# Kernel tuning notes

Hardware: AMD Instinct MI355X
Metric: run time of the kernel (lower is better)

## Reference

```python
import jax, jax.numpy as jnp
import numpy as np

N = 100000   # nodes
E = 600000   # edges
K = 3        # TAGConv hops
EPS = 1e-5   # BatchNorm eps
SLOPE = 0.01 # LeakyReLU negative slope


def setup_inputs() -> dict:
    key = jax.random.key(0)
    ks = jax.random.split(key, 8)
    y = jax.random.normal(ks[0], (N, 128), dtype=jnp.float32)
    edge_index = jax.random.randint(ks[1], (2, E), 0, N, dtype=jnp.int64)
    edge_attr = jax.random.uniform(ks[2], (E,), dtype=jnp.float32)
    # TAGConv layer l has (K+1) weight matrices [in, out]; bias only on first two layers
    W1 = 0.1 * jax.random.normal(ks[3], (K + 1, 128, 128), dtype=jnp.float32)
    b1 = jnp.full((128,), 0.1, dtype=jnp.float32)
    W2 = 0.1 * jax.random.normal(ks[4], (K + 1, 128, 128), dtype=jnp.float32)
    b2 = jnp.full((128,), 0.1, dtype=jnp.float32)
    W3 = 0.1 * jax.random.normal(ks[5], (K + 1, 128, 64), dtype=jnp.float32)
    g1 = jnp.ones((128,), jnp.float32); be1 = jnp.zeros((128,), jnp.float32)
    g2 = jnp.ones((128,), jnp.float32); be2 = jnp.zeros((128,), jnp.float32)
    g3 = jnp.ones((64,), jnp.float32);  be3 = jnp.zeros((64,), jnp.float32)
    return dict(y=y, edge_index=edge_index, edge_attr=edge_attr,
                W1=W1, b1=b1, g1=g1, be1=be1,
                W2=W2, b2=b2, g2=g2, be2=be2,
                W3=W3, g3=g3, be3=be3)


def _tag_conv(x, W, b, src, dst, norm):
    # out = sum_{k=0..K} A_hat^k x @ W_k (+ b)
    out = x @ W[0]
    h = x
    for k in range(1, W.shape[0]):
        h = jax.ops.segment_sum(norm[:, None] * h[src], dst, num_segments=N)
        out = out + h @ W[k]
    return out if b is None else out + b


def _bn(x, g, b):
    # BatchNorm1d training mode: biased batch stats over nodes
    m = x.mean(axis=0)
    v = jnp.mean((x - m) ** 2, axis=0)
    return (x - m) * jax.lax.rsqrt(v + EPS) * g + b


def reference(y, edge_index, edge_attr, W1, b1, g1, be1, W2, b2, g2, be2, W3, g3, be3):
    src, dst = edge_index[0], edge_index[1]
    # gcn_norm (symmetric, no self-loops): D^{-1/2} A D^{-1/2}
    deg = jax.ops.segment_sum(edge_attr, dst, num_segments=N)
    dis = jnp.where(deg > 0, jax.lax.rsqrt(jnp.maximum(deg, 1e-12)), 0.0)
    norm = dis[src] * edge_attr * dis[dst]
    lrelu = lambda t: jax.nn.leaky_relu(t, SLOPE)
    x = lrelu(_bn(_tag_conv(y, W1, b1, src, dst, norm), g1, be1))
    x = lrelu(_bn(_tag_conv(x, W2, b2, src, dst, norm), g2, be2))
    x = lrelu(_bn(_tag_conv(x, W3, None, src, dst, norm), g3, be3))
    return x
```

## Files before the change

kernel.cpp:

```cpp
#include <hip/hip_runtime.h>
#include <hip/hip_bf16.h>

typedef unsigned short b16;
typedef __attribute__((ext_vector_type(8))) unsigned short us8;
typedef __attribute__((ext_vector_type(8))) short short8;
typedef __attribute__((ext_vector_type(4))) float float4v;

#define NN 100000
#define NE 600000

__device__ __forceinline__ float bf2f(b16 u) {
    return __uint_as_float(((unsigned)u) << 16);
}
__device__ __forceinline__ b16 f2bf(float f) {
    unsigned x = __float_as_uint(f);
    return (b16)((x + 0x7fffu + ((x >> 16) & 1u)) >> 16);
}

__global__ void k_detect(const void* __restrict__ y, const void* __restrict__ ei,
                         int* __restrict__ flags) {
    if (threadIdx.x == 0 && blockIdx.x == 0) {
        const b16* p = (const b16*)y;
        int f32 = 0;
        for (int i = 0; i < 128; ++i) {
            float v = bf2f(p[i]);
            if (!(fabsf(v) < 1e4f)) { f32 = 1; break; }
        }
        flags[0] = f32;
        const long long* q = (const long long*)ei;
        int i64 = 1;
        for (int i = 0; i < 4; ++i) {
            long long v = q[i];
            if (v < 0 || v >= NN) i64 = 0;
        }
        flags[1] = i64;
    }
}

__global__ void k_cvt(const void* __restrict__ in, float* __restrict__ out, int n,
                      const int* __restrict__ flags) {
    int i = blockIdx.x * blockDim.x + threadIdx.x;
    if (i >= n) return;
    out[i] = flags[0] ? ((const float*)in)[i] : bf2f(((const b16*)in)[i]);
}

__global__ void k_idx(const void* __restrict__ ei, int* __restrict__ src32,
                      int* __restrict__ dst32, const int* __restrict__ flags) {
    int e = blockIdx.x * blockDim.x + threadIdx.x;
    if (e >= NE) return;
    int s, d;
    if (flags[1]) {
        const long long* p = (const long long*)ei;
        s = (int)p[e];
        d = (int)p[NE + e];
    } else {
        const int* p = (const int*)ei;
        s = p[e];
        d = p[NE + e];
    }
    src32[e] = ((unsigned)s < NN) ? s : 0;
    dst32[e] = ((unsigned)d < NN) ? d : 0;
}

__global__ void k_degcnt(const int* __restrict__ dst, const void* __restrict__ ea,
                         float* __restrict__ deg, int* __restrict__ cnt,
                         const int* __restrict__ flags) {
    int e = blockIdx.x * blockDim.x + threadIdx.x;
    if (e >= NE) return;
    float w = flags[0] ? ((const float*)ea)[e] : bf2f(((const b16*)ea)[e]);
    int d = dst[e];
    unsafeAtomicAdd(&deg[d], w);
    atomicAdd(&cnt[d], 1);
}

__global__ void k_dis(float* deg) {
    int n = blockIdx.x * blockDim.x + threadIdx.x;
    if (n < NN) {
        float d = deg[n];
        deg[n] = (d > 0.f) ? rsqrtf(fmaxf(d, 1e-12f)) : 0.f;
    }
}

#define SCAN_B 1024
#define SCAN_NB ((NN + SCAN_B - 1) / SCAN_B)

__global__ __launch_bounds__(SCAN_B) void k_scan1(const int* __restrict__ cnt,
                                                  int* __restrict__ inc,
                                                  int* __restrict__ bsum) {
    __shared__ int s[SCAN_B];
    int i = blockIdx.x * SCAN_B + threadIdx.x;
    s[threadIdx.x] = (i < NN) ? cnt[i] : 0;
    __syncthreads();
    for (int off = 1; off < SCAN_B; off <<= 1) {
        int t = (threadIdx.x >= off) ? s[threadIdx.x - off] : 0;
        __syncthreads();
        s[threadIdx.x] += t;
        __syncthreads();
    }
    if (i < NN) inc[i] = s[threadIdx.x];
    if (threadIdx.x == SCAN_B - 1) bsum[blockIdx.x] = s[SCAN_B - 1];
}

__global__ void k_scan2(int* bsum) {
    if (threadIdx.x == 0 && blockIdx.x == 0) {
        int a = 0;
        for (int i = 0; i < SCAN_NB; ++i) {
            int t = bsum[i];
            bsum[i] = a;
            a += t;
        }
    }
}

__global__ void k_scan3(const int* __restrict__ inc, const int* __restrict__ bsum,
                        int* __restrict__ rowptr) {
    int i = blockIdx.x * blockDim.x + threadIdx.x;
    if (i == 0) rowptr[0] = 0;
    if (i < NN) rowptr[i + 1] = inc[i] + bsum[i / SCAN_B];
}

__global__ void k_fill(const int* __restrict__ src, const int* __restrict__ dst,
                       const void* __restrict__ ea, const float* __restrict__ dis,
                       const int* __restrict__ rowptr, int* __restrict__ fill,
                       int* __restrict__ csrc, float* __restrict__ cw,
                       const int* __restrict__ flags) {
    int e = blockIdx.x * blockDim.x + threadIdx.x;
    if (e >= NE) return;
    float a = flags[0] ? ((const float*)ea)[e] : bf2f(((const b16*)ea)[e]);
    int d = dst[e];
    int s = src[e];
    int pos = rowptr[d] + atomicAdd(&fill[d], 1);
    csrc[pos] = s;
    cw[pos] = dis[s] * a * dis[d];
}

__global__ void k_pack(const void* __restrict__ W, b16* __restrict__ Wp, int NC,
                       const int* __restrict__ flags) {
    int f = blockIdx.x * blockDim.x + threadIdx.x;
    int total = 512 * NC / 8;
    if (f >= total) return;
    int lane = f & 63;
    int rest = f >> 6;
    int CT = NC >> 4;
    int ct = rest % CT, ks = rest / CT;
    int k0 = 32 * ks + (lane >> 4) * 8;
    int col = 16 * ct + (lane & 15);
    us8 v;
#pragma unroll
    for (int j = 0; j < 8; ++j) {
        float x = flags[0] ? ((const float*)W)[(size_t)(k0 + j) * NC + col]
                           : bf2f(((const b16*)W)[(size_t)(k0 + j) * NC + col]);
        v[j] = f2bf(x);
    }
    *(us8*)&Wp[(size_t)f * 8] = v;
}

__global__ void k_cast(const void* __restrict__ y, b16* __restrict__ XC,
                       const int* __restrict__ flags) {
    int i = blockIdx.x * blockDim.x + threadIdx.x;
    if (i >= NN * 32) return;
    int row = i >> 5, cg = i & 31;
    float4 v;
    if (flags[0]) {
        v = ((const float4*)y)[i];
    } else {
        ushort4 u = ((const ushort4*)y)[i];
        v = make_float4(bf2f(u.x), bf2f(u.y), bf2f(u.z), bf2f(u.w));
    }
    ushort4 o;
    o.x = f2bf(v.x); o.y = f2bf(v.y); o.z = f2bf(v.z); o.w = f2bf(v.w);
    *(ushort4*)&XC[(size_t)row * 512 + 4 * cg] = o;
}

__global__ __launch_bounds__(256) void k_spmm(b16* __restrict__ XC, int ci, int co,
                                              const int* __restrict__ rowptr,
                                              const int* __restrict__ csrc,
                                              const float* __restrict__ cw) {
    int gid = blockIdx.x * blockDim.x + threadIdx.x;
    int node = gid >> 6;
    if (node >= NN) return;
    int lane = gid & 63;
    int grp = lane >> 4;
    int l15 = lane & 15;
    int beg = rowptr[node], end = rowptr[node + 1];

    float a0[8], a1[8];
#pragma unroll
    for (int j = 0; j < 8; ++j) {
        a0[j] = 0.f;
        a1[j] = 0.f;
    }
    for (int i = beg; i < end; i += 16) {
        int e0 = i + grp, e1 = i + 4 + grp, e2 = i + 8 + grp, e3 = i + 12 + grp;
        float w0 = (e0 < end) ? cw[e0] : 0.f;
        float w1 = (e1 < end) ? cw[e1] : 0.f;
        float w2 = (e2 < end) ? cw[e2] : 0.f;
        float w3 = (e3 < end) ? cw[e3] : 0.f;
        int lim = end - 1;
        int s0 = csrc[e0 < lim ? e0 : lim];
        int s1 = csrc[e1 < lim ? e1 : lim];
        int s2 = csrc[e2 < lim ? e2 : lim];
        int s3 = csrc[e3 < lim ? e3 : lim];
        us8 u0 = *(const us8*)&XC[(size_t)s0 * 512 + ci + 8 * l15];
        us8 u1 = *(const us8*)&XC[(size_t)s1 * 512 + ci + 8 * l15];
        us8 u2 = *(const us8*)&XC[(size_t)s2 * 512 + ci + 8 * l15];
        us8 u3 = *(const us8*)&XC[(size_t)s3 * 512 + ci + 8 * l15];
#pragma unroll
        for (int j = 0; j < 8; ++j) {
            a0[j] = fmaf(w0, bf2f(u0[j]), a0[j]);
            a1[j] = fmaf(w1, bf2f(u1[j]), a1[j]);
            a0[j] = fmaf(w2, bf2f(u2[j]), a0[j]);
            a1[j] = fmaf(w3, bf2f(u3[j]), a1[j]);
        }
    }
#pragma unroll
    for (int j = 0; j < 8; ++j) a0[j] += a1[j];
#pragma unroll
    for (int j = 0; j < 8; ++j) a0[j] += __shfl_xor(a0[j], 16);
#pragma unroll
    for (int j = 0; j < 8; ++j) a0[j] += __shfl_xor(a0[j], 32);
    if (grp == 0) {
        us8 o;
#pragma unroll
        for (int j = 0; j < 8; ++j) o[j] = f2bf(a0[j]);
        *(us8*)&XC[(size_t)node * 512 + co + 8 * l15] = o;
    }
}

template <int NC>
__global__ __launch_bounds__(256) void k_mgemm(const b16* __restrict__ XC,
                                               const b16* __restrict__ Wp,
                                               const float* __restrict__ bias,
                                               b16* __restrict__ OUT,
                                               float* __restrict__ gsum,
                                               float* __restrict__ gsq) {
    constexpr int CT = NC / 16;
    __shared__ float csum[NC], csq[NC];
    const int tid = threadIdx.x;
    const int wave = tid >> 6;
    const int lane = tid & 63;
    const int quad = lane >> 4;
    const int l15 = lane & 15;
    const int rbase = blockIdx.x * 128 + wave * 32;

    for (int i = tid; i < NC; i += 256) {
        csum[i] = 0.f;
        csq[i] = 0.f;
    }

    float4v acc[2][CT];
#pragma unroll
    for (int rt = 0; rt < 2; ++rt)
#pragma unroll
        for (int ct = 0; ct < CT; ++ct) acc[rt][ct] = (float4v)(0.f);

    const b16* gA[2];
#pragma unroll
    for (int rt = 0; rt < 2; ++rt) {
        int r = rbase + 16 * rt + l15;
        if (r >= NN) r = NN - 1;
        gA[rt] = XC + (size_t)r * 512 + quad * 8;
    }
    const b16* gB = Wp + lane * 8;

    short8 afc[2], bfc[CT], afn[2], bfn[CT];
#pragma unroll
    for (int rt = 0; rt < 2; ++rt) afc[rt] = *(const short8*)(gA[rt]);
#pragma unroll
    for (int ct = 0; ct < CT; ++ct) bfc[ct] = *(const short8*)(gB + ct * 512);

    for (int ks = 0; ks < 16; ++ks) {
        if (ks < 15) {
#pragma unroll
            for (int rt = 0; rt < 2; ++rt)
                afn[rt] = *(const short8*)(gA[rt] + 32 * (ks + 1));
#pragma unroll
            for (int ct = 0; ct < CT; ++ct)
                bfn[ct] = *(const short8*)(gB + (size_t)((ks + 1) * CT + ct) * 512);
        }
#pragma unroll
        for (int rt = 0; rt < 2; ++rt)
#pragma unroll
            for (int ct = 0; ct < CT; ++ct)
                acc[rt][ct] = __builtin_amdgcn_mfma_f32_16x16x32_bf16(
                    afc[rt], bfc[ct], acc[rt][ct], 0, 0, 0);
        if (ks < 15) {
#pragma unroll
            for (int rt = 0; rt < 2; ++rt) afc[rt] = afn[rt];
#pragma unroll
            for (int ct = 0; ct < CT; ++ct) bfc[ct] = bfn[ct];
        }
    }

#pragma unroll
    for (int rt = 0; rt < 2; ++rt) {
#pragma unroll
        for (int ct = 0; ct < CT; ++ct) {
            int col = 16 * ct + l15;
            float bv = bias ? bias[col] : 0.f;
            float s = 0.f, sq = 0.f;
#pragma unroll
            for (int r = 0; r < 4; ++r) {
                int row = rbase + 16 * rt + quad * 4 + r;
                if (row < NN) {
                    float v = acc[rt][ct][r] + bv;
                    OUT[(size_t)row * NC + col] = f2bf(v);
                    s += v;
                    sq += v * v;
                }
            }
            s += __shfl_xor(s, 16);
            s += __shfl_xor(s, 32);
            sq += __shfl_xor(sq, 16);
            sq += __shfl_xor(sq, 32);
            if (quad == 0) {
                atomicAdd(&csum[col], s);
                atomicAdd(&csq[col], sq);
            }
        }
    }
    __syncthreads();
    for (int i = tid; i < NC; i += 256) {
        unsafeAtomicAdd(&gsum[i], csum[i]);
        unsafeAtomicAdd(&gsq[i], csq[i]);
    }
}

__global__ void k_bnparam(const float* gsum, const float* gsq, const float* g,
                          const float* be, float* scale, float* shift, int ncols) {
    int c = threadIdx.x;
    if (c < ncols) {
        float m = gsum[c] * (1.f / NN);
        float v = gsq[c] * (1.f / NN) - m * m;
        v = fmaxf(v, 0.f);
        float s = rsqrtf(v + 1e-5f) * g[c];
        scale[c] = s;
        shift[c] = be[c] - m * s;
    }
}

__global__ void k_bnapply_mid(const b16* __restrict__ OUT,
                              const float* __restrict__ scale,
                              const float* __restrict__ shift, b16* __restrict__ XC) {
    int i = blockIdx.x * blockDim.x + threadIdx.x;
    if (i >= NN * 64) return;
    int row = i >> 6, c = (i & 63) * 2;
    ushort2 u = *(const ushort2*)&OUT[(size_t)row * 128 + c];
    float a = fmaf(bf2f(u.x), scale[c], shift[c]);
    float b = fmaf(bf2f(u.y), scale[c + 1], shift[c + 1]);
    a = a > 0.f ? a : 0.01f * a;
    b = b > 0.f ? b : 0.01f * b;
    ushort2 o;
    o.x = f2bf(a);
    o.y = f2bf(b);
    *(ushort2*)&XC[(size_t)row * 512 + c] = o;
}

__global__ void k_bnapply_last(const b16* __restrict__ OUT,
                               const float* __restrict__ scale,
                               const float* __restrict__ shift, void* __restrict__ dout,
                               const int* __restrict__ flags) {
    int i = blockIdx.x * blockDim.x + threadIdx.x;
    if (i >= NN * 64) return;
    int c = i & 63;
    float v = fmaf(bf2f(OUT[i]), scale[c], shift[c]);
    v = v > 0.f ? v : 0.01f * v;
    if (flags[0])
        ((float*)dout)[i] = v;
    else
        ((b16*)dout)[i] = f2bf(v);
}

#define PB_B1 0
#define PB_B2 128
#define PB_G1 256
#define PB_BE1 384
#define PB_G2 512
#define PB_BE2 640
#define PB_G3 768
#define PB_BE3 832
#define PB_SZ 896

extern "C" void kernel_launch(void* const* d_in, const int* in_sizes, int n_in,
                              void* d_out, int out_size, void* d_ws, size_t ws_size,
                              hipStream_t stream) {
    const void* y   = d_in[0];
    const void* ei  = d_in[1];
    const void* ea  = d_in[2];
    const void* W1  = d_in[3];
    const void* b1  = d_in[4];
    const void* g1  = d_in[5];
    const void* be1 = d_in[6];
    const void* W2  = d_in[7];
    const void* b2  = d_in[8];
    const void* g2  = d_in[9];
    const void* be2 = d_in[10];
    const void* W3  = d_in[11];
    const void* g3  = d_in[12];
    const void* be3 = d_in[13];

    char* w = (char*)d_ws;
    size_t used = 0;
    auto carve = [&](size_t bytes) -> char* {
        char* p = w + used;
        used += (bytes + 255) & ~(size_t)255;
        return p;
    };

    int* flags   = (int*)carve(16);
    int* src32   = (int*)carve((size_t)NE * 4);
    int* dst32   = (int*)carve((size_t)NE * 4);
    float* deg   = (float*)carve((size_t)NN * 4);
    int* cnt     = (int*)carve((size_t)NN * 4);
    int* rowptr  = (int*)carve((size_t)(NN + 1) * 4);
    int* cscan   = (int*)carve((size_t)NN * 4);
    int* bsum    = (int*)carve((size_t)SCAN_NB * 4);
    int* csrc    = (int*)carve((size_t)NE * 4);
    float* cw    = (float*)carve((size_t)NE * 4);
    float* PB    = (float*)carve(PB_SZ * 4);
    b16* Wp1     = (b16*)carve((size_t)512 * 128 * 2);
    b16* Wp2     = (b16*)carve((size_t)512 * 128 * 2);
    b16* Wp3     = (b16*)carve((size_t)512 * 64 * 2);
    b16* OUT     = (b16*)carve((size_t)NN * 128 * 2);
    float* gsum  = (float*)carve(128 * 4);
    float* gsq   = (float*)carve(128 * 4);
    float* scale = (float*)carve(128 * 4);
    float* shift = (float*)carve(128 * 4);
    b16* XC      = (b16*)carve((size_t)NN * 512 * 2);

    k_detect<<<1, 64, 0, stream>>>(y, ei, flags);
    auto cvt = [&](const void* in, float* out, int n) {
        k_cvt<<<(n + 127) / 128, 128, 0, stream>>>(in, out, n, flags);
    };
    cvt(b1, PB + PB_B1, 128);
    cvt(b2, PB + PB_B2, 128);
    cvt(g1, PB + PB_G1, 128);
    cvt(be1, PB + PB_BE1, 128);
    cvt(g2, PB + PB_G2, 128);
    cvt(be2, PB + PB_BE2, 128);
    cvt(g3, PB + PB_G3, 64);
    cvt(be3, PB + PB_BE3, 64);
    k_pack<<<(512 * 128 / 8 + 255) / 256, 256, 0, stream>>>(W1, Wp1, 128, flags);
    k_pack<<<(512 * 128 / 8 + 255) / 256, 256, 0, stream>>>(W2, Wp2, 128, flags);
    k_pack<<<(512 * 64 / 8 + 255) / 256, 256, 0, stream>>>(W3, Wp3, 64, flags);

    k_idx<<<(NE + 255) / 256, 256, 0, stream>>>(ei, src32, dst32, flags);
    hipMemsetAsync(deg, 0, (size_t)NN * 4, stream);
    hipMemsetAsync(cnt, 0, (size_t)NN * 4, stream);
    k_degcnt<<<(NE + 255) / 256, 256, 0, stream>>>(dst32, ea, deg, cnt, flags);
    k_dis<<<(NN + 255) / 256, 256, 0, stream>>>(deg);
    k_scan1<<<SCAN_NB, SCAN_B, 0, stream>>>(cnt, cscan, bsum);
    k_scan2<<<1, 64, 0, stream>>>(bsum);
    k_scan3<<<(NN + 255) / 256, 256, 0, stream>>>(cscan, bsum, rowptr);
    hipMemsetAsync(cnt, 0, (size_t)NN * 4, stream);
    k_fill<<<(NE + 255) / 256, 256, 0, stream>>>(src32, dst32, ea, deg, rowptr, cnt,
                                                 csrc, cw, flags);

    k_cast<<<(NN * 32 + 255) / 256, 256, 0, stream>>>(y, XC, flags);

    auto spmm = [&](int ci, int co) {
        k_spmm<<<(NN * 64 + 255) / 256, 256, 0, stream>>>(XC, ci, co, rowptr, csrc, cw);
    };
    const int gemm_grid = (NN + 127) / 128;

    auto layer = [&](const b16* Wp, const float* bias, const float* g, const float* be,
                     int NC, bool last) {
        spmm(0, 128);
        spmm(128, 256);
        spmm(256, 384);
        hipMemsetAsync(gsum, 0, NC * 4, stream);
        hipMemsetAsync(gsq, 0, NC * 4, stream);
        if (NC == 128)
            k_mgemm<128><<<gemm_grid, 256, 0, stream>>>(XC, Wp, bias, OUT, gsum, gsq);
        else
            k_mgemm<64><<<gemm_grid, 256, 0, stream>>>(XC, Wp, bias, OUT, gsum, gsq);
        k_bnparam<<<1, NC, 0, stream>>>(gsum, gsq, g, be, scale, shift, NC);
        if (last)
            k_bnapply_last<<<(NN * 64 + 255) / 256, 256, 0, stream>>>(OUT, scale, shift,
                                                                      d_out, flags);
        else
            k_bnapply_mid<<<(NN * 64 + 255) / 256, 256, 0, stream>>>(OUT, scale, shift,
                                                                     XC);
    };

    layer(Wp1, PB + PB_B1, PB + PB_G1, PB + PB_BE1, 128, false);
    layer(Wp2, PB + PB_B2, PB + PB_G2, PB + PB_BE2, 128, false);
    layer(Wp3, nullptr, PB + PB_G3, PB + PB_BE3, 64, true);
}
```

Before: 791.4 us.

## Remap SpMM lanes to columns and retile fused GEMM into 64x64 per-wave tiles

The SpMM kernel now gives each of the 64 lanes two feature columns and walks every edge of the row sequentially, four at a time. This removes the cross-group shuffle reduction and the masked-off lanes on short rows, at the cost of fewer independent gathers in flight per lane. The GEMM kernel now splits output columns across blockIdx.y in 64-column slices and computes a 64x64 tile per wave with double-buffered register fragments. This raises MFMA work per fragment load, but A-row reads are repeated for each column slice and register pressure grows.

```diff
diff --git a/kernel.cpp b/kernel.cpp
--- a/kernel.cpp
+++ b/kernel.cpp
@@ -180,123 +180,111 @@
     int node = gid >> 6;
     if (node >= NN) return;
     int lane = gid & 63;
-    int grp = lane >> 4;
-    int l15 = lane & 15;
     int beg = rowptr[node], end = rowptr[node + 1];
-
-    float a0[8], a1[8];
-#pragma unroll
-    for (int j = 0; j < 8; ++j) {
-        a0[j] = 0.f;
-        a1[j] = 0.f;
-    }
-    for (int i = beg; i < end; i += 16) {
-        int e0 = i + grp, e1 = i + 4 + grp, e2 = i + 8 + grp, e3 = i + 12 + grp;
-        float w0 = (e0 < end) ? cw[e0] : 0.f;
+    int coff = ci + 2 * lane;
+
+    float ax0 = 0.f, ay0 = 0.f, ax1 = 0.f, ay1 = 0.f;
+    for (int i = beg; i < end; i += 4) {
+        int lim = end - 1;
+        int e1 = i + 1, e2 = i + 2, e3 = i + 3;
+        float w0 = cw[i];
         float w1 = (e1 < end) ? cw[e1] : 0.f;
         float w2 = (e2 < end) ? cw[e2] : 0.f;
         float w3 = (e3 < end) ? cw[e3] : 0.f;
-        int lim = end - 1;
-        int s0 = csrc[e0 < lim ? e0 : lim];
+        int s0 = csrc[i];
         int s1 = csrc[e1 < lim ? e1 : lim];
         int s2 = csrc[e2 < lim ? e2 : lim];
         int s3 = csrc[e3 < lim ? e3 : lim];
-        us8 u0 = *(const us8*)&XC[(size_t)s0 * 512 + ci + 8 * l15];
-        us8 u1 = *(const us8*)&XC[(size_t)s1 * 512 + ci + 8 * l15];
-        us8 u2 = *(const us8*)&XC[(size_t)s2 * 512 + ci + 8 * l15];
-        us8 u3 = *(const us8*)&XC[(size_t)s3 * 512 + ci + 8 * l15];
-#pragma unroll
-        for (int j = 0; j < 8; ++j) {
-            a0[j] = fmaf(w0, bf2f(u0[j]), a0[j]);
-            a1[j] = fmaf(w1, bf2f(u1[j]), a1[j]);
-            a0[j] = fmaf(w2, bf2f(u2[j]), a0[j]);
-            a1[j] = fmaf(w3, bf2f(u3[j]), a1[j]);
-        }
-    }
-#pragma unroll
-    for (int j = 0; j < 8; ++j) a0[j] += a1[j];
-#pragma unroll
-    for (int j = 0; j < 8; ++j) a0[j] += __shfl_xor(a0[j], 16);
-#pragma unroll
-    for (int j = 0; j < 8; ++j) a0[j] += __shfl_xor(a0[j], 32);
-    if (grp == 0) {
-        us8 o;
-#pragma unroll
-        for (int j = 0; j < 8; ++j) o[j] = f2bf(a0[j]);
-        *(us8*)&XC[(size_t)node * 512 + co + 8 * l15] = o;
-    }
-}
-
-template <int NC>
+        unsigned u0 = *(const unsigned*)&XC[(size_t)s0 * 512 + coff];
+        unsigned u1 = *(const unsigned*)&XC[(size_t)s1 * 512 + coff];
+        unsigned u2 = *(const unsigned*)&XC[(size_t)s2 * 512 + coff];
+        unsigned u3 = *(const unsigned*)&XC[(size_t)s3 * 512 + coff];
+        ax0 = fmaf(w0, __uint_as_float(u0 << 16), ax0);
+        ay0 = fmaf(w0, __uint_as_float(u0 & 0xFFFF0000u), ay0);
+        ax1 = fmaf(w1, __uint_as_float(u1 << 16), ax1);
+        ay1 = fmaf(w1, __uint_as_float(u1 & 0xFFFF0000u), ay1);
+        ax0 = fmaf(w2, __uint_as_float(u2 << 16), ax0);
+        ay0 = fmaf(w2, __uint_as_float(u2 & 0xFFFF0000u), ay0);
+        ax1 = fmaf(w3, __uint_as_float(u3 << 16), ax1);
+        ay1 = fmaf(w3, __uint_as_float(u3 & 0xFFFF0000u), ay1);
+    }
+    ax0 += ax1;
+    ay0 += ay1;
+    ushort2 o;
+    o.x = f2bf(ax0);
+    o.y = f2bf(ay0);
+    *(ushort2*)&XC[(size_t)node * 512 + co + 2 * lane] = o;
+}
+
+template <int CTF>
 __global__ __launch_bounds__(256) void k_mgemm(const b16* __restrict__ XC,
                                                const b16* __restrict__ Wp,
                                                const float* __restrict__ bias,
                                                b16* __restrict__ OUT,
                                                float* __restrict__ gsum,
                                                float* __restrict__ gsq) {
-    constexpr int CT = NC / 16;
-    __shared__ float csum[NC], csq[NC];
+    constexpr int NC = CTF * 16;
+    __shared__ float csum[64], csq[64];
     const int tid = threadIdx.x;
     const int wave = tid >> 6;
     const int lane = tid & 63;
     const int quad = lane >> 4;
     const int l15 = lane & 15;
-    const int rbase = blockIdx.x * 128 + wave * 32;
-
-    for (int i = tid; i < NC; i += 256) {
+    const int cb = blockIdx.y;
+    const int cbase = cb * 4;
+    const int rbase = blockIdx.x * 256 + wave * 64;
+
+    for (int i = tid; i < 64; i += 256) {
         csum[i] = 0.f;
         csq[i] = 0.f;
     }
 
-    float4v acc[2][CT];
-#pragma unroll
-    for (int rt = 0; rt < 2; ++rt)
-#pragma unroll
-        for (int ct = 0; ct < CT; ++ct) acc[rt][ct] = (float4v)(0.f);
-
-    const b16* gA[2];
-#pragma unroll
-    for (int rt = 0; rt < 2; ++rt) {
+    float4v acc[4][4];
+#pragma unroll
+    for (int rt = 0; rt < 4; ++rt)
+#pragma unroll
+        for (int ct = 0; ct < 4; ++ct) acc[rt][ct] = (float4v)(0.f);
+
+    const b16* gA[4];
+#pragma unroll
+    for (int rt = 0; rt < 4; ++rt) {
         int r = rbase + 16 * rt + l15;
         if (r >= NN) r = NN - 1;
         gA[rt] = XC + (size_t)r * 512 + quad * 8;
     }
-    const b16* gB = Wp + lane * 8;
-
-    short8 afc[2], bfc[CT], afn[2], bfn[CT];
-#pragma unroll
-    for (int rt = 0; rt < 2; ++rt) afc[rt] = *(const short8*)(gA[rt]);
-#pragma unroll
-    for (int ct = 0; ct < CT; ++ct) bfc[ct] = *(const short8*)(gB + ct * 512);
-
+    const b16* gB = Wp + (size_t)cbase * 512 + lane * 8;
+
+    short8 ab[2][4], bb[2][4];
+#pragma unroll
+    for (int rt = 0; rt < 4; ++rt) ab[0][rt] = *(const short8*)(gA[rt]);
+#pragma unroll
+    for (int ct = 0; ct < 4; ++ct) bb[0][ct] = *(const short8*)(gB + ct * 512);
+
+#pragma unroll
     for (int ks = 0; ks < 16; ++ks) {
+        const int cur = ks & 1, nxt = cur ^ 1;
         if (ks < 15) {
 #pragma unroll
-            for (int rt = 0; rt < 2; ++rt)
-                afn[rt] = *(const short8*)(gA[rt] + 32 * (ks + 1));
-#pragma unroll
-            for (int ct = 0; ct < CT; ++ct)
-                bfn[ct] = *(const short8*)(gB + (size_t)((ks + 1) * CT + ct) * 512);
+            for (int rt = 0; rt < 4; ++rt)
+                ab[nxt][rt] = *(const short8*)(gA[rt] + 32 * (ks + 1));
+#pragma unroll
+            for (int ct = 0; ct < 4; ++ct)
+                bb[nxt][ct] = *(const short8*)(gB + (size_t)(ks + 1) * CTF * 512 + ct * 512);
         }
 #pragma unroll
-        for (int rt = 0; rt < 2; ++rt)
-#pragma unroll
-            for (int ct = 0; ct < CT; ++ct)
+        for (int rt = 0; rt < 4; ++rt)
+#pragma unroll
+            for (int ct = 0; ct < 4; ++ct)
                 acc[rt][ct] = __builtin_amdgcn_mfma_f32_16x16x32_bf16(
-                    afc[rt], bfc[ct], acc[rt][ct], 0, 0, 0);
-        if (ks < 15) {
-#pragma unroll
-            for (int rt = 0; rt < 2; ++rt) afc[rt] = afn[rt];
-#pragma unroll
-            for (int ct = 0; ct < CT; ++ct) bfc[ct] = bfn[ct];
-        }
-    }
-
-#pragma unroll
-    for (int rt = 0; rt < 2; ++rt) {
-#pragma unroll
-        for (int ct = 0; ct < CT; ++ct) {
-            int col = 16 * ct + l15;
+                    ab[cur][rt], bb[cur][ct], acc[rt][ct], 0, 0, 0);
+    }
+
+#pragma unroll
+    for (int rt = 0; rt < 4; ++rt) {
+#pragma unroll
+        for (int ct = 0; ct < 4; ++ct) {
+            int cl = 16 * ct + l15;
+            int col = cb * 64 + cl;
             float bv = bias ? bias[col] : 0.f;
             float s = 0.f, sq = 0.f;
 #pragma unroll
@@ -314,15 +302,15 @@
             sq += __shfl_xor(sq, 16);
             sq += __shfl_xor(sq, 32);
             if (quad == 0) {
-                atomicAdd(&csum[col], s);
-                atomicAdd(&csq[col], sq);
+                atomicAdd(&csum[cl], s);
+                atomicAdd(&csq[cl], sq);
             }
         }
     }
     __syncthreads();
-    for (int i = tid; i < NC; i += 256) {
-        unsafeAtomicAdd(&gsum[i], csum[i]);
-        unsafeAtomicAdd(&gsq[i], csq[i]);
+    if (tid < 64) {
+        unsafeAtomicAdd(&gsum[cb * 64 + tid], csum[tid]);
+        unsafeAtomicAdd(&gsq[cb * 64 + tid], csq[tid]);
     }
 }
 
@@ -461,7 +449,7 @@
     auto spmm = [&](int ci, int co) {
         k_spmm<<<(NN * 64 + 255) / 256, 256, 0, stream>>>(XC, ci, co, rowptr, csrc, cw);
     };
-    const int gemm_grid = (NN + 127) / 128;
+    const int gemm_gx = (NN + 255) / 256;
 
     auto layer = [&](const b16* Wp, const float* bias, const float* g, const float* be,
                      int NC, bool last) {
@@ -471,9 +459,9 @@
         hipMemsetAsync(gsum, 0, NC * 4, stream);
         hipMemsetAsync(gsq, 0, NC * 4, stream);
         if (NC == 128)
-            k_mgemm<128><<<gemm_grid, 256, 0, stream>>>(XC, Wp, bias, OUT, gsum, gsq);
+            k_mgemm<8><<<dim3(gemm_gx, 2), 256, 0, stream>>>(XC, Wp, bias, OUT, gsum, gsq);
         else
-            k_mgemm<64><<<gemm_grid, 256, 0, stream>>>(XC, Wp, bias, OUT, gsum, gsq);
+            k_mgemm<4><<<dim3(gemm_gx, 1), 256, 0, stream>>>(XC, Wp, bias, OUT, gsum, gsq);
         k_bnparam<<<1, NC, 0, stream>>>(gsum, gsq, g, be, scale, shift, NC);
         if (last)
             k_bnapply_last<<<(NN * 64 + 255) / 256, 256, 0, stream>>>(OUT, scale, shift,
```

New measurement: 819.8 us. 3.6% more time.
